# Kernel optimization log

Hardware: AMD Instinct MI355X
Metric: run time of the kernel (lower is better)

Reference implementation:

```python
import jax, jax.numpy as jnp
import numpy as np
import math

B, L = 4096, 16
W_TC = 2.0  # forward arg w_tc; default 1.0 makes the loss identically 0, so use 2.0
LOG_2PI = math.log(2.0 * math.pi)


def gaussian_log_density(samples, mean, log_var):
    # elementwise Gaussian log-density; broadcasts to [B, B, L]
    inv_sigma = jnp.exp(-log_var)
    tmp = samples - mean
    return -0.5 * (tmp * tmp * inv_sigma + log_var + LOG_2PI)


def setup_inputs() -> dict:
    key = jax.random.key(0)
    k1, k2, k3 = jax.random.split(key, 3)
    z = jax.random.normal(k1, (B, L), dtype=jnp.float32)
    z_mean = jax.random.normal(k2, (B, L), dtype=jnp.float32)
    z_logvar = jax.random.normal(k3, (B, L), dtype=jnp.float32)
    return {"z": z, "z_mean": z_mean, "z_logvar": z_logvar}


def reference(z, z_mean, z_logvar):
    # log q(z_i(sample) | x_j) per latent dim: [B_sample, B_dist, L]
    log_qz_prob = gaussian_log_density(z[:, None, :], z_mean[None, :, :], z_logvar[None, :, :])
    # log prod_l (sum_j exp(.)) : logsumexp over distribution axis, sum over latent axis
    # (original computes exp().sum().log(); logsumexp is the same math, stabilized)
    log_qz_product = jnp.sum(jax.nn.logsumexp(log_qz_prob, axis=1), axis=1)  # [B]
    # log sum_j exp( sum_l log q ) : sum over latent axis first, logsumexp over dists
    log_qz = jax.nn.logsumexp(jnp.sum(log_qz_prob, axis=2), axis=1)  # [B]
    return (W_TC - 1.0) * jnp.mean(log_qz - log_qz_product)
```

## Files before the change

kernel.cpp:

```cpp
#include <hip/hip_runtime.h>
#include <math.h>

#define B_N 4096
#define L_N 16
#define NJC 64
#define R_I 4
#define IPB 256
#define NW  4
#define JT  64
#define JPW (JT / NW)

#define NHALF_LOG2E 0.7213475204444817f
#define LOG2E_F     1.4426950408889634f
#define LN2_F       0.6931471805599453f
#define LOG_2PI_F   1.8378770664093453f

typedef float f32x2 __attribute__((ext_vector_type(2)));

#define LDSF (NW * 17 * 128)


extern "C" __global__ __launch_bounds__(256, 3)
void btc_main(const float* __restrict__ z, const float* __restrict__ zm,
              const float* __restrict__ zlv, float* __restrict__ part,
              int jc ) {
    __shared__ __align__(16) float lds[LDSF];
    float* sA = lds;
    float* sB = lds + JT * L_N;
    float* sC = lds + 2 * JT * L_N;
    float (*red)[17][128] = (float (*)[17][128])lds;

    const int tid  = threadIdx.x;
    const int lane = tid & 63;
    const int w    = tid >> 6;

    f32x2 zr[R_I][8], acc[R_I][8];
    float sum2[R_I];
    #pragma unroll
    for (int r = 0; r < R_I; ++r) {
        const float4* zp = (const float4*)(z + (size_t)(blockIdx.x * IPB + r * 64 + lane) * L_N);
        #pragma unroll
        for (int q = 0; q < 4; ++q) {
            float4 v = zp[q];
            zr[r][2*q]   = (f32x2){v.x, v.y};
            zr[r][2*q+1] = (f32x2){v.z, v.w};
            acc[r][2*q]   = (f32x2){0.f, 0.f};
            acc[r][2*q+1] = (f32x2){0.f, 0.f};
        }
        sum2[r] = 0.0f;
    }

    for (int t = 0; t < jc / JT; ++t) {
        __syncthreads();
        const size_t gbase = ((size_t)blockIdx.y * jc + (size_t)t * JT) * L_N;
        {
            const int e4 = tid * 4;
            float4 m4 = *(const float4*)(zm  + gbase + e4);
            float4 v4 = *(const float4*)(zlv + gbase + e4);
            float4 a4, b4, c4;
            float A;
            A = -NHALF_LOG2E * __builtin_amdgcn_exp2f(-LOG2E_F * v4.x);
            a4.x = A; b4.x = -2.0f * A * m4.x;
            c4.x = fmaf(A, m4.x * m4.x, -NHALF_LOG2E * (v4.x + LOG_2PI_F));
            A = -NHALF_LOG2E * __builtin_amdgcn_exp2f(-LOG2E_F * v4.y);
            a4.y = A; b4.y = -2.0f * A * m4.y;
            c4.y = fmaf(A, m4.y * m4.y, -NHALF_LOG2E * (v4.y + LOG_2PI_F));
            A = -NHALF_LOG2E * __builtin_amdgcn_exp2f(-LOG2E_F * v4.z);
            a4.z = A; b4.z = -2.0f * A * m4.z;
            c4.z = fmaf(A, m4.z * m4.z, -NHALF_LOG2E * (v4.z + LOG_2PI_F));
            A = -NHALF_LOG2E * __builtin_amdgcn_exp2f(-LOG2E_F * v4.w);
            a4.w = A; b4.w = -2.0f * A * m4.w;
            c4.w = fmaf(A, m4.w * m4.w, -NHALF_LOG2E * (v4.w + LOG_2PI_F));
            *(float4*)&sA[e4] = a4;
            *(float4*)&sB[e4] = b4;
            *(float4*)&sC[e4] = c4;
        }
        __syncthreads();

        for (int jj = 0; jj < JPW; ++jj) {
            const int jo = (w * JPW + jj) * L_N;
            const float4* pA = (const float4*)&sA[jo];
            const float4* pB = (const float4*)&sB[jo];
            const float4* pC = (const float4*)&sC[jo];
            f32x2 s2[R_I];
            #pragma unroll
            for (int r = 0; r < R_I; ++r) s2[r] = (f32x2){0.f, 0.f};
            #pragma unroll
            for (int q = 0; q < 4; ++q) {
                float4 A4 = pA[q], B4 = pB[q], C4 = pC[q];
                f32x2 A0 = {A4.x, A4.y}, A1 = {A4.z, A4.w};
                f32x2 B0 = {B4.x, B4.y}, B1 = {B4.z, B4.w};
                f32x2 C0 = {C4.x, C4.y}, C1 = {C4.z, C4.w};
                #pragma unroll
                for (int r = 0; r < R_I; ++r) {
                    f32x2 tv, lg;
                    tv = A0 * zr[r][2*q] + B0;  lg = tv * zr[r][2*q] + C0;  s2[r] += lg;
                    acc[r][2*q]   += (f32x2){__builtin_amdgcn_exp2f(lg.x), __builtin_amdgcn_exp2f(lg.y)};
                    tv = A1 * zr[r][2*q+1] + B1; lg = tv * zr[r][2*q+1] + C1; s2[r] += lg;
                    acc[r][2*q+1] += (f32x2){__builtin_amdgcn_exp2f(lg.x), __builtin_amdgcn_exp2f(lg.y)};
                }
            }
            #pragma unroll
            for (int r = 0; r < R_I; ++r)
                sum2[r] += __builtin_amdgcn_exp2f(s2[r].x + s2[r].y);
        }
    }

    float* bbase = part + (size_t)blockIdx.y * 17 * B_N + blockIdx.x * IPB;
    #pragma unroll
    for (int p = 0; p < 2; ++p) {
        __syncthreads();
        #pragma unroll
        for (int q = 0; q < 8; ++q) {
            red[w][2*q][lane]          = acc[2*p][q].x;
            red[w][2*q + 1][lane]      = acc[2*p][q].y;
            red[w][2*q][64 + lane]     = acc[2*p + 1][q].x;
            red[w][2*q + 1][64 + lane] = acc[2*p + 1][q].y;
        }
        red[w][16][lane]      = sum2[2*p];
        red[w][16][64 + lane] = sum2[2*p + 1];
        __syncthreads();
        if (tid < 128) {
            #pragma unroll
            for (int f = 0; f < 17; ++f) {
                float v = (red[0][f][tid] + red[1][f][tid]) +
                          (red[2][f][tid] + red[3][f][tid]);
                bbase[(size_t)f * B_N + p * 128 + tid] = v;
            }
        }
    }
}

extern "C" __global__ __launch_bounds__(256)
void btc_sum(const float* __restrict__ part, float* __restrict__ part2,
             float* __restrict__ out, int njc) {
    const int g = blockIdx.x * 256 + threadIdx.x;
    if (g == 0) out[0] = 0.0f;
    float s = 0.0f;
    for (int c = 0; c < njc; ++c) s += part[(size_t)c * 17 * B_N + g];
    part2[g] = s;
}

extern "C" __global__ __launch_bounds__(256)
void btc_fin(const float* __restrict__ part2, float* __restrict__ out) {
    const int tid = threadIdx.x;
    const int i   = blockIdx.x * 256 + tid;

    float lqprod2 = 0.0f;
    #pragma unroll
    for (int l = 0; l < L_N; ++l)
        lqprod2 += __builtin_amdgcn_logf(part2[(size_t)l * B_N + i]);
    float v = LN2_F * (__builtin_amdgcn_logf(part2[(size_t)16 * B_N + i]) - lqprod2);

    #pragma unroll
    for (int off = 32; off > 0; off >>= 1) v += __shfl_down(v, off);
    __shared__ float red[4];
    const int lane = tid & 63, w = tid >> 6;
    if (lane == 0) red[w] = v;
    __syncthreads();
    if (tid == 0)
        atomicAdd(out, ((red[0] + red[1]) + (red[2] + red[3])) * (1.0f / (float)B_N));
}

extern "C" void kernel_launch(void* const* d_in, const int* in_sizes, int n_in,
                              void* d_out, int out_size, void* d_ws, size_t ws_size,
                              hipStream_t stream) {
    const float* z   = (const float*)d_in[0];
    const float* zm  = (const float*)d_in[1];
    const float* zlv = (const float*)d_in[2];
    float* out  = (float*)d_out;
    float* part = (float*)d_ws;

    int njc = NJC;
    while (njc > 1) {
        size_t need = ((size_t)njc * 17 * B_N + 17 * B_N) * sizeof(float);
        if (need <= ws_size) break;
        njc >>= 1;
    }
    const int jc = B_N / njc;
    float* part2 = part + (size_t)njc * 17 * B_N;

    hipLaunchKernelGGL(btc_main, dim3(B_N / IPB, njc), dim3(256), 0, stream,
                       z, zm, zlv, part, jc);
    hipLaunchKernelGGL(btc_sum, dim3(17 * B_N / 256), dim3(256), 0, stream,
                       part, part2, out, njc);
    hipLaunchKernelGGL(btc_fin, dim3(B_N / 256), dim3(256), 0, stream,
                       part2, out);
}
```

Before: 57.19 us.

## Replace joint-density exp with product of per-dim exps and halve rows per thread

```diff
diff --git a/kernel.cpp b/kernel.cpp
--- a/kernel.cpp
+++ b/kernel.cpp
@@ -4,8 +4,8 @@
 #define B_N 4096
 #define L_N 16
 #define NJC 64
-#define R_I 4
-#define IPB 256
+#define R_I 2
+#define IPB 128
 #define NW  4
 #define JT  64
 #define JPW (JT / NW)
@@ -17,10 +17,10 @@
 
 typedef float f32x2 __attribute__((ext_vector_type(2)));
 
-#define LDSF (NW * 17 * 128)
+#define LDSF (NW * 17 * 64)
 
 
-extern "C" __global__ __launch_bounds__(256, 3)
+extern "C" __global__ __launch_bounds__(256, 5)
 void btc_main(const float* __restrict__ z, const float* __restrict__ zm,
               const float* __restrict__ zlv, float* __restrict__ part,
               int jc ) {
@@ -28,7 +28,7 @@
     float* sA = lds;
     float* sB = lds + JT * L_N;
     float* sC = lds + 2 * JT * L_N;
-    float (*red)[17][128] = (float (*)[17][128])lds;
+    float (*red)[17][64] = (float (*)[17][64])lds;
 
     const int tid  = threadIdx.x;
     const int lane = tid & 63;
@@ -82,9 +82,9 @@
             const float4* pA = (const float4*)&sA[jo];
             const float4* pB = (const float4*)&sB[jo];
             const float4* pC = (const float4*)&sC[jo];
-            f32x2 s2[R_I];
+            f32x2 prod[R_I];
             #pragma unroll
-            for (int r = 0; r < R_I; ++r) s2[r] = (f32x2){0.f, 0.f};
+            for (int r = 0; r < R_I; ++r) prod[r] = (f32x2){1.f, 1.f};
             #pragma unroll
             for (int q = 0; q < 4; ++q) {
                 float4 A4 = pA[q], B4 = pB[q], C4 = pC[q];
@@ -93,39 +93,38 @@
                 f32x2 C0 = {C4.x, C4.y}, C1 = {C4.z, C4.w};
                 #pragma unroll
                 for (int r = 0; r < R_I; ++r) {
-                    f32x2 tv, lg;
-                    tv = A0 * zr[r][2*q] + B0;  lg = tv * zr[r][2*q] + C0;  s2[r] += lg;
-                    acc[r][2*q]   += (f32x2){__builtin_amdgcn_exp2f(lg.x), __builtin_amdgcn_exp2f(lg.y)};
-                    tv = A1 * zr[r][2*q+1] + B1; lg = tv * zr[r][2*q+1] + C1; s2[r] += lg;
-                    acc[r][2*q+1] += (f32x2){__builtin_amdgcn_exp2f(lg.x), __builtin_amdgcn_exp2f(lg.y)};
+                    f32x2 tv, lg, e;
+                    tv = A0 * zr[r][2*q] + B0;  lg = tv * zr[r][2*q] + C0;
+                    e  = (f32x2){__builtin_amdgcn_exp2f(lg.x), __builtin_amdgcn_exp2f(lg.y)};
+                    acc[r][2*q] += e;  prod[r] *= e;
+                    tv = A1 * zr[r][2*q+1] + B1; lg = tv * zr[r][2*q+1] + C1;
+                    e  = (f32x2){__builtin_amdgcn_exp2f(lg.x), __builtin_amdgcn_exp2f(lg.y)};
+                    acc[r][2*q+1] += e;  prod[r] *= e;
                 }
             }
             #pragma unroll
             for (int r = 0; r < R_I; ++r)
-                sum2[r] += __builtin_amdgcn_exp2f(s2[r].x + s2[r].y);
+                sum2[r] += prod[r].x * prod[r].y;
         }
     }
 
     float* bbase = part + (size_t)blockIdx.y * 17 * B_N + blockIdx.x * IPB;
     #pragma unroll
-    for (int p = 0; p < 2; ++p) {
+    for (int r = 0; r < R_I; ++r) {
         __syncthreads();
         #pragma unroll
         for (int q = 0; q < 8; ++q) {
-            red[w][2*q][lane]          = acc[2*p][q].x;
-            red[w][2*q + 1][lane]      = acc[2*p][q].y;
-            red[w][2*q][64 + lane]     = acc[2*p + 1][q].x;
-            red[w][2*q + 1][64 + lane] = acc[2*p + 1][q].y;
+            red[w][2*q][lane]     = acc[r][q].x;
+            red[w][2*q + 1][lane] = acc[r][q].y;
         }
-        red[w][16][lane]      = sum2[2*p];
-        red[w][16][64 + lane] = sum2[2*p + 1];
+        red[w][16][lane] = sum2[r];
         __syncthreads();
-        if (tid < 128) {
+        if (tid < 64) {
             #pragma unroll
             for (int f = 0; f < 17; ++f) {
                 float v = (red[0][f][tid] + red[1][f][tid]) +
                           (red[2][f][tid] + red[3][f][tid]);
-                bbase[(size_t)f * B_N + p * 128 + tid] = v;
+                bbase[(size_t)f * B_N + r * 64 + tid] = v;
             }
         }
     }
```

After: 66.68 us. +16.6%, slower.
